# Optimization experiments

Measured on AMD Instinct MI355X. Metric: run time of the kernel, lower is better.

## Reference

```python
import jax, jax.numpy as jnp
import numpy as np
from jax import lax

B, S, D = 4, 2048, 1024
E, F, K = 8, 2816, 2
W_SCALE = 0.02


def setup_inputs() -> dict:
    key = jax.random.key(0)
    ks = jax.random.split(key, 5)
    return {
        "x": jax.random.normal(ks[0], (B, S, D), dtype=jnp.float32),
        "gate_w": jax.random.normal(ks[1], (E, D), dtype=jnp.float32) * W_SCALE,
        "w_gate": jax.random.normal(ks[2], (E, F, D), dtype=jnp.float32) * W_SCALE,
        "w_up": jax.random.normal(ks[3], (E, F, D), dtype=jnp.float32) * W_SCALE,
        "w_down": jax.random.normal(ks[4], (E, D, F), dtype=jnp.float32) * W_SCALE,
    }


def reference(x, gate_w, w_gate, w_up, w_down):
    # Router: logits [B,S,E]
    logits = jnp.einsum("bsd,ed->bse", x, gate_w)
    top_v, top_i = lax.top_k(logits, K)              # [B,S,K]
    top_w = jax.nn.softmax(top_v, axis=-1)           # [B,S,K]
    probs = jax.nn.softmax(logits, axis=-1)
    expert_usage = probs.mean(axis=(0, 1))           # [E]
    aux_loss = ((expert_usage - 1.0 / E) ** 2).sum()

    # Per-token per-expert combine weight: cw[b,s,e] = sum_k top_w[...,k] * 1[top_i[...,k]==e]
    onehot = jax.nn.one_hot(top_i, E, dtype=x.dtype)       # [B,S,K,E]
    cw = jnp.einsum("bsk,bske->ebs", top_w, onehot)        # [E,B,S]

    # Loop (scan) over the small fixed expert axis; each expert: SwiGLU FFN over all
    # tokens, masked/weighted by cw (same math as masked gather + scatter-add combine).
    def body(acc, ew):
        wg, wu, wd, cwe = ew                                # [F,D],[F,D],[D,F],[B,S]
        g = jax.nn.silu(jnp.einsum("bsd,fd->bsf", x, wg))
        u = jnp.einsum("bsd,fd->bsf", x, wu)
        out_e = jnp.einsum("bsf,df->bsd", g * u, wd)
        return acc + cwe[..., None] * out_e, None

    out, _ = lax.scan(body, jnp.zeros_like(x), (w_gate, w_up, w_down, cw))
    return out, aux_loss
```

## Files before the change

### kernel.cpp

```cpp
#include <hip/hip_runtime.h>
#include <hip/hip_bf16.h>
#include <stdint.h>

#define Dd 1024
#define Ee 8
#define Ff 2816
#define Tt 8192
#define Pp 16384

#define BMT 128
#define MAXT 136

using bf16x8 = __attribute__((ext_vector_type(8))) short;
using f32x4  = __attribute__((ext_vector_type(4))) float;
using f4v    = __attribute__((ext_vector_type(4))) float;
using u4v    = __attribute__((ext_vector_type(4))) unsigned int;

__device__ __forceinline__ uint16_t f2bf(float f) {
    union { float f; uint32_t u; } v; v.f = f;
    return (uint16_t)((v.u + 0x7fffu + ((v.u >> 16) & 1u)) >> 16);
}
__device__ __forceinline__ float bf2f(uint16_t b) {
    union { uint32_t u; float f; } v; v.u = (uint32_t)b << 16; return v.f;
}
__device__ __forceinline__ uint32_t pack2(float a, float b) {
    return (uint32_t)f2bf(a) | ((uint32_t)f2bf(b) << 16);
}
__device__ __forceinline__ u4v pack8v(f4v a, f4v b) {
    u4v r; r.x = pack2(a.x, a.y); r.y = pack2(a.z, a.w);
    r.z = pack2(b.x, b.y); r.w = pack2(b.z, b.w); return r;
}
__device__ __forceinline__ int swz(int row, int cb) {
    return row * 128 + (cb ^ ((row & 7) << 4));
}
__device__ __forceinline__ void gload16(const void* g, void* lds) {
    __builtin_amdgcn_global_load_lds(
        (const __attribute__((address_space(1))) uint32_t*)(uintptr_t)g,
        (__attribute__((address_space(3))) uint32_t*)(uintptr_t)lds,
        16, 0, 0);
}

__global__ __launch_bounds__(256) void router_kernel(
    const float* __restrict__ x, const float* __restrict__ gw,
    float* __restrict__ usage_part, int* __restrict__ tok_i,
    float* __restrict__ tok_w, uint16_t* __restrict__ Xb)
{
    __shared__ float usw[4][Ee];
    int tid = threadIdx.x;
    int wave = tid >> 6, lane = tid & 63;
    int t = blockIdx.x * 4 + wave;

    const float* xp = x + (size_t)t * Dd + lane * 16;
    f4v xr0 = *(const f4v*)(xp);
    f4v xr1 = *(const f4v*)(xp + 4);
    f4v xr2 = *(const f4v*)(xp + 8);
    f4v xr3 = *(const f4v*)(xp + 12);

    uint4* dst = (uint4*)(Xb + (size_t)t * Dd + lane * 16);
    u4v p0 = pack8v(xr0, xr1), p1 = pack8v(xr2, xr3);
    dst[0] = *(uint4*)&p0;
    dst[1] = *(uint4*)&p1;

    float logits[Ee];
    #pragma unroll
    for (int e = 0; e < Ee; ++e) {
        const float* gp = gw + e * Dd + lane * 16;
        f4v g0 = *(const f4v*)(gp);
        f4v g1 = *(const f4v*)(gp + 4);
        f4v g2 = *(const f4v*)(gp + 8);
        f4v g3 = *(const f4v*)(gp + 12);
        f4v sv = xr0 * g0 + xr1 * g1 + xr2 * g2 + xr3 * g3;
        float s = sv.x + sv.y + sv.z + sv.w;
        #pragma unroll
        for (int m = 1; m < 64; m <<= 1) s += __shfl_xor(s, m, 64);
        logits[e] = s;
    }
    float v1 = -1e30f, v2 = -1e30f; int i1 = 0, i2 = 0;
    #pragma unroll
    for (int e = 0; e < Ee; ++e) {
        float l = logits[e];
        if (l > v1) { v2 = v1; i2 = i1; v1 = l; i1 = e; }
        else if (l > v2) { v2 = l; i2 = e; }
    }
    float ex2 = expf(v2 - v1);
    float w1 = 1.f / (1.f + ex2);
    float w2 = ex2 * w1;
    float p[Ee]; float se = 0.f;
    #pragma unroll
    for (int e = 0; e < Ee; ++e) { p[e] = expf(logits[e] - v1); se += p[e]; }
    float inv = 1.f / se;
    if (lane == 0) {
        #pragma unroll
        for (int e = 0; e < Ee; ++e) usw[wave][e] = p[e] * inv;
        tok_i[t * 2] = i1; tok_i[t * 2 + 1] = i2;
        tok_w[t * 2] = w1; tok_w[t * 2 + 1] = w2;
    }
    __syncthreads();
    if (tid < Ee)
        usage_part[(size_t)blockIdx.x * Ee + tid] =
            usw[0][tid] + usw[1][tid] + usw[2][tid] + usw[3][tid];
}

__global__ __launch_bounds__(256) void hist_kernel(
    const int* __restrict__ tok_i, int* __restrict__ hist)
{
    __shared__ int h[Ee];
    int tid = threadIdx.x;
    if (tid < Ee) h[tid] = 0;
    __syncthreads();
    int t = blockIdx.x * 256 + tid;
    atomicAdd(&h[tok_i[t * 2]], 1);
    atomicAdd(&h[tok_i[t * 2 + 1]], 1);
    __syncthreads();
    if (tid < Ee) hist[blockIdx.x * Ee + tid] = h[tid];
}

__global__ void scan_kernel(
    const float* __restrict__ usage_part, const int* __restrict__ hist,
    int* __restrict__ seg_off, int* __restrict__ boff, int* __restrict__ ntiles,
    int* __restrict__ tile_e, int* __restrict__ tile_row0, float* __restrict__ out_aux)
{
    __shared__ float us[Ee][32];
    int tid = threadIdx.x;
    int e = tid & 7, sl = tid >> 3;
    float s = 0.f;
    for (int b = sl; b < Tt / 4; b += 32) s += usage_part[(size_t)b * Ee + e];
    us[e][sl] = s;
    __syncthreads();
    if (tid == 0) {
        float aux = 0.f;
        int counts[Ee];
        for (int ee = 0; ee < Ee; ++ee) {
            float u = 0.f;
            for (int k = 0; k < 32; ++k) u += us[ee][k];
            u /= (float)Tt;
            float d = u - 0.125f; aux += d * d;
        }
        *out_aux = aux;
        for (int ee = 0; ee < Ee; ++ee) {
            int c = 0;
            for (int b2 = 0; b2 < 32; ++b2) c += hist[b2 * Ee + ee];
            counts[ee] = c;
        }
        int off = 0;
        for (int ee = 0; ee < Ee; ++ee) { seg_off[ee] = off; off += counts[ee]; }
        seg_off[Ee] = off;
        int cur[Ee];
        for (int ee = 0; ee < Ee; ++ee) cur[ee] = seg_off[ee];
        for (int b2 = 0; b2 < 32; ++b2)
            for (int ee = 0; ee < Ee; ++ee) {
                boff[b2 * Ee + ee] = cur[ee];
                cur[ee] += hist[b2 * Ee + ee];
            }
        int ti = 0;
        for (int ee = 0; ee < Ee; ++ee) {
            int so = seg_off[ee], cnt = counts[ee];
            for (int r = 0; r < cnt; r += BMT) { tile_e[ti] = ee; tile_row0[ti] = so + r; ++ti; }
        }
        *ntiles = ti;
    }
}

__global__ __launch_bounds__(256) void emit_kernel(
    const int* __restrict__ tok_i, const float* __restrict__ tok_w,
    const int* __restrict__ boff, int* __restrict__ token_id,
    float* __restrict__ pair_w, int* __restrict__ pos)
{
    __shared__ int cur[Ee];
    int tid = threadIdx.x;
    if (tid < Ee) cur[tid] = boff[blockIdx.x * Ee + tid];
    __syncthreads();
    int t = blockIdx.x * 256 + tid;
    int i1 = tok_i[t * 2], i2 = tok_i[t * 2 + 1];
    int s1 = atomicAdd(&cur[i1], 1);
    token_id[s1] = t; pair_w[s1] = tok_w[t * 2];     pos[t * 2] = s1;
    int s2 = atomicAdd(&cur[i2], 1);
    token_id[s2] = t; pair_w[s2] = tok_w[t * 2 + 1]; pos[t * 2 + 1] = s2;
}

__global__ __launch_bounds__(256) void conv_all_kernel(
    const float* __restrict__ g, const float* __restrict__ u,
    const float* __restrict__ dsrc, uint16_t* __restrict__ w1b,
    uint16_t* __restrict__ wdb)
{
    int part = blockIdx.x / 1408;
    long long base = (long long)(blockIdx.x - part * 1408) * 16384;
    int tid = threadIdx.x;
    const float* src = (part == 0) ? g : (part == 1) ? u : dsrc;
    f4v v[16];
    #pragma unroll
    for (int j = 0; j < 8; ++j) {
        const float* s = src + base + j * 2048 + tid * 8;
        v[2 * j]     = __builtin_nontemporal_load((const f4v*)s);
        v[2 * j + 1] = __builtin_nontemporal_load((const f4v*)(s + 4));
    }
    __builtin_amdgcn_sched_barrier(0);
    if (part == 2) {
        #pragma unroll
        for (int j = 0; j < 8; ++j) {
            long long ii = base + j * 2048 + tid * 8;
            *(u4v*)(wdb + ii) = pack8v(v[2 * j], v[2 * j + 1]);
        }
    } else {
        int roff = (part == 1) ? 16 : 0;
        #pragma unroll
        for (int j = 0; j < 8; ++j) {
            long long ii = base + j * 2048 + tid * 8;
            int d = (int)(ii & 1023);
            long long row = ii >> 10;
            int e = (int)(row / Ff), f = (int)(row - (long long)e * Ff);
            size_t rg = (size_t)e * 5632 + (size_t)(f >> 4) * 32 + (f & 15) + roff;
            *(u4v*)(w1b + rg * 1024 + d) = pack8v(v[2 * j], v[2 * j + 1]);
        }
    }
}

template<int NKT, int MODE>
__device__ __forceinline__ void gemm_core(
    const uint16_t* __restrict__ Abase, const uint16_t* __restrict__ Bbase,
    const int* __restrict__ seg_off, const int* __restrict__ tile_e,
    const int* __restrict__ tile_row0, const int* __restrict__ ntiles,
    const int* __restrict__ token_id, const float* __restrict__ pair_w,
    uint16_t* __restrict__ hbuf, uint16_t* __restrict__ Pbuf, float* __restrict__ out,
    int tile0, int Tc, int ltr)
{
    constexpr int LD = (MODE == 0) ? Dd : Ff;

    int b = blockIdx.x;
    int nt, lt;
    if constexpr (MODE == 0) {
        int x = b & 7, p = b >> 3;
        nt = p / ltr;
        lt = x * ltr + (p - nt * ltr);
        if (lt >= Tc) return;
    } else {
        nt = b & 7;
        lt = b >> 3;
    }
    int tidx = tile0 + lt;
    if (tidx >= *ntiles) return;
    int e = tile_e[tidx];
    int row0 = tile_row0[tidx];
    int rows = seg_off[e + 1] - row0; if (rows > BMT) rows = BMT;
    int slot = lt * BMT;

    __shared__ uint4 lds4[32768 / 16];
    char* smA = (char*)lds4;
    char* smB = smA + 16384;

    int tid = threadIdx.x, lane = tid & 63, wv = tid >> 6;
    int wr = wv >> 1, wc = wv & 1;

    int srow = wv * 32 + (lane >> 3);
    int csw = ((lane & 7) ^ (lane >> 3)) * 8;
    const uint16_t* aPs[4];
    const uint16_t* bP;
    if constexpr (MODE == 0) {
        #pragma unroll
        for (int i = 0; i < 4; ++i) {
            int pr = row0 + srow + i * 8;
            if (pr > Pp - 1) pr = Pp - 1;
            aPs[i] = Abase + (size_t)token_id[pr] * Dd + csw;
        }
        bP = Bbase + ((size_t)e * 5632 + nt * 128 + srow) * LD + csw;
    } else {
        const uint16_t* aP0 = Abase + (size_t)(slot + srow) * LD + csw;
        #pragma unroll
        for (int i = 0; i < 4; ++i) aPs[i] = aP0 + (size_t)(i * 8) * LD;
        bP = Bbase + ((size_t)e * Dd + nt * 128 + srow) * LD + csw;
    }
    char* aL = smA + wv * 4096;
    char* bL = smB + wv * 4096;

    f32x4 acc[4][4];
    f32x4 zero4 = {0.f, 0.f, 0.f, 0.f};
    #pragma unroll
    for (int m = 0; m < 4; ++m)
        #pragma unroll
        for (int n = 0; n < 4; ++n) acc[m][n] = zero4;

    #pragma unroll 1
    for (int kt = 0; kt < NKT; ++kt) {
        #pragma unroll
        for (int i = 0; i < 4; ++i) {
            gload16(aPs[i] + kt * 64, aL + i * 1024);
            gload16(bP + (size_t)(i * 8) * LD + kt * 64, bL + i * 1024);
        }
        __syncthreads();
        #pragma unroll
        for (int kk = 0; kk < 2; ++kk) {
            int cb = kk * 64 + ((lane >> 4) << 4);
            bf16x8 a[4], bfr[4];
            #pragma unroll
            for (int m = 0; m < 4; ++m)
                a[m] = *(const bf16x8*)(smA + swz(wr * 64 + m * 16 + (lane & 15), cb));
            #pragma unroll
            for (int n = 0; n < 4; ++n)
                bfr[n] = *(const bf16x8*)(smB + swz(wc * 64 + n * 16 + (lane & 15), cb));
            #pragma unroll
            for (int m = 0; m < 4; ++m)
                #pragma unroll
                for (int n = 0; n < 4; ++n)
                    acc[m][n] = __builtin_amdgcn_mfma_f32_16x16x32_bf16(a[m], bfr[n], acc[m][n], 0, 0, 0);
        }
        __syncthreads();
    }

    if constexpr (MODE == 0) {
        int hc = nt * 64 + wc * 32 + (lane & 15);
        #pragma unroll
        for (int m = 0; m < 4; ++m) {
            #pragma unroll
            for (int g = 0; g < 4; ++g) {
                int rr = wr * 64 + m * 16 + (lane >> 4) * 4 + g;
                if (rr < rows) {
                    uint16_t* hp = hbuf + (size_t)(slot + rr) * Ff + hc;
                    float g0 = acc[m][0][g], u0 = acc[m][1][g];
                    hp[0]  = f2bf(g0 * u0 / (1.f + expf(-g0)));
                    float g1 = acc[m][2][g], u1 = acc[m][3][g];
                    hp[16] = f2bf(g1 * u1 / (1.f + expf(-g1)));
                }
            }
        }
    } else if constexpr (MODE == 1) {
        int col = nt * 128 + wc * 64 + (lane & 15);
        #pragma unroll
        for (int m = 0; m < 4; ++m) {
            #pragma unroll
            for (int g = 0; g < 4; ++g) {
                int rr = wr * 64 + m * 16 + (lane >> 4) * 4 + g;
                if (rr < rows) {
                    uint16_t* pp = Pbuf + (size_t)(row0 + rr) * Dd + col;
                    pp[0]  = f2bf(acc[m][0][g]);
                    pp[16] = f2bf(acc[m][1][g]);
                    pp[32] = f2bf(acc[m][2][g]);
                    pp[48] = f2bf(acc[m][3][g]);
                }
            }
        }
    } else {
        int col = nt * 128 + wc * 64 + (lane & 15);
        #pragma unroll
        for (int m = 0; m < 4; ++m) {
            #pragma unroll
            for (int g = 0; g < 4; ++g) {
                int rr = wr * 64 + m * 16 + (lane >> 4) * 4 + g;
                if (rr < rows) {
                    int pr = row0 + rr;
                    int tok = token_id[pr];
                    float w = pair_w[pr];
                    float* op = out + (size_t)tok * Dd + col;
                    atomicAdd(op + 0,  w * acc[m][0][g]);
                    atomicAdd(op + 16, w * acc[m][1][g]);
                    atomicAdd(op + 32, w * acc[m][2][g]);
                    atomicAdd(op + 48, w * acc[m][3][g]);
                }
            }
        }
    }
}

#define GEMM_ARGS const uint16_t* __restrict__ Abase, const uint16_t* __restrict__ Bbase, \
    const int* __restrict__ seg_off, const int* __restrict__ tile_e, \
    const int* __restrict__ tile_row0, const int* __restrict__ ntiles, \
    const int* __restrict__ token_id, const float* __restrict__ pair_w, \
    uint16_t* __restrict__ hbuf, uint16_t* __restrict__ Pbuf, float* __restrict__ out, \
    int tile0, int Tc, int ltr
#define GEMM_PASS Abase, Bbase, seg_off, tile_e, tile_row0, ntiles, token_id, pair_w, \
    hbuf, Pbuf, out, tile0, Tc, ltr

__global__ __launch_bounds__(256, 3) void gemm1_kernel(GEMM_ARGS) {
    gemm_core<16, 0>(GEMM_PASS);
}
__global__ __launch_bounds__(256, 3) void gemm2p_kernel(GEMM_ARGS) {
    gemm_core<44, 1>(GEMM_PASS);
}
__global__ __launch_bounds__(256, 3) void gemm2a_kernel(GEMM_ARGS) {
    gemm_core<44, 2>(GEMM_PASS);
}

__global__ __launch_bounds__(256) void combine_kernel(
    const uint16_t* __restrict__ P, const int* __restrict__ pos,
    const float* __restrict__ tok_w, float* __restrict__ out)
{
    int t = blockIdx.x;
    int d = threadIdx.x * 4;
    int s1 = pos[t * 2], s2 = pos[t * 2 + 1];
    float w1 = tok_w[t * 2], w2 = tok_w[t * 2 + 1];
    uint2 pa = *(const uint2*)(P + (size_t)s1 * Dd + d);
    uint2 pb = *(const uint2*)(P + (size_t)s2 * Dd + d);
    f4v o;
    o.x = w1 * bf2f((uint16_t)(pa.x & 0xffff))  + w2 * bf2f((uint16_t)(pb.x & 0xffff));
    o.y = w1 * bf2f((uint16_t)(pa.x >> 16))     + w2 * bf2f((uint16_t)(pb.x >> 16));
    o.z = w1 * bf2f((uint16_t)(pa.y & 0xffff))  + w2 * bf2f((uint16_t)(pb.y & 0xffff));
    o.w = w1 * bf2f((uint16_t)(pa.y >> 16))     + w2 * bf2f((uint16_t)(pb.y >> 16));
    *(f4v*)(out + (size_t)t * Dd + d) = o;
}

extern "C" void kernel_launch(void* const* d_in, const int* in_sizes, int n_in,
                              void* d_out, int out_size, void* d_ws, size_t ws_size,
                              hipStream_t stream)
{
    const float* x     = (const float*)d_in[0];
    const float* gw    = (const float*)d_in[1];
    const float* wgate = (const float*)d_in[2];
    const float* wup   = (const float*)d_in[3];
    const float* wdown = (const float*)d_in[4];
    float* out = (float*)d_out;

    char* ws = (char*)d_ws;
    float* usage_part = (float*)(ws);
    int*   hist       = (int*)(ws + 65536);
    int*   seg_off    = (int*)(ws + 66560);
    int*   boff       = (int*)(ws + 66624);
    int*   ntiles     = (int*)(ws + 67648);
    int*   tile_e     = (int*)(ws + 67712);
    int*   tile_row0  = (int*)(ws + 68736);
    int*   tok_i      = (int*)(ws + 73728);
    float* tok_w      = (float*)(ws + 139264);
    int*   token_id   = (int*)(ws + 204800);
    float* pair_w     = (float*)(ws + 270336);
    int*   pos        = (int*)(ws + 335872);
    const size_t CTRL  = 401408;
    const size_t TILEB = (size_t)BMT * Ff * 2;
    const size_t XbB   = (size_t)Tt * Dd * 2;
    const size_t W1B   = 2ull * Ee * Ff * Dd * 2;
    const size_t WDB   = (size_t)Ee * Dd * Ff * 2;
    const size_t PB    = (size_t)Pp * Dd * 2;

    size_t fixed = CTRL + XbB + W1B + WDB;
    if (ws_size < fixed + TILEB) {
        hipMemsetAsync(d_out, 0, (size_t)out_size * 4, stream);
        return;
    }

    uint16_t* Xb   = (uint16_t*)(ws + CTRL);
    uint16_t* W1b  = (uint16_t*)(ws + CTRL + XbB);
    uint16_t* wd_b = (uint16_t*)(ws + CTRL + XbB + W1B);
    size_t rem = ws_size - fixed;

    router_kernel<<<Tt / 4, 256, 0, stream>>>(x, gw, usage_part, tok_i, tok_w, Xb);
    hist_kernel<<<Tt / 256, 256, 0, stream>>>(tok_i, hist);
    scan_kernel<<<1, 256, 0, stream>>>(usage_part, hist, seg_off, boff,
                                       ntiles, tile_e, tile_row0, out + (out_size - 1));
    emit_kernel<<<Tt / 256, 256, 0, stream>>>(tok_i, tok_w, boff, token_id, pair_w, pos);
    conv_all_kernel<<<3 * 1408, 256, 0, stream>>>(wgate, wup, wdown, W1b, wd_b);

    int TcP = (rem > PB) ? (int)((rem - PB) / TILEB) : 0;
    if (TcP > MAXT) TcP = MAXT;
    bool useP = (TcP >= 24);
    uint16_t* Pbuf = nullptr;
    uint16_t* hbuf;
    int Tc;
    if (useP) {
        Pbuf = (uint16_t*)(ws + fixed);
        hbuf = (uint16_t*)(ws + fixed + PB);
        Tc = TcP;
    } else {
        hbuf = (uint16_t*)(ws + fixed);
        Tc = (int)(rem / TILEB);
        if (Tc > MAXT) Tc = MAXT;
        hipMemsetAsync(d_out, 0, (size_t)(out_size - 1) * 4, stream);
    }
    int nchunks = (MAXT + Tc - 1) / Tc;
    Tc = (MAXT + nchunks - 1) / nchunks;

    int ltr = (Tc + 7) / 8;
    int nwg1 = 8 * ltr * 44;
    int nwg2 = Tc * 8;
    for (int c = 0; c < nchunks; ++c) {
        int tile0 = c * Tc;
        gemm1_kernel<<<nwg1, 256, 0, stream>>>(
            Xb, W1b, seg_off, tile_e, tile_row0, ntiles, token_id, pair_w,
            hbuf, Pbuf, out, tile0, Tc, ltr);
        if (useP) {
            gemm2p_kernel<<<nwg2, 256, 0, stream>>>(
                hbuf, wd_b, seg_off, tile_e, tile_row0, ntiles, token_id, pair_w,
                hbuf, Pbuf, out, tile0, Tc, ltr);
        } else {
            gemm2a_kernel<<<nwg2, 256, 0, stream>>>(
                hbuf, wd_b, seg_off, tile_e, tile_row0, ntiles, token_id, pair_w,
                hbuf, Pbuf, out, tile0, Tc, ltr);
        }
    }
    if (useP)
        combine_kernel<<<Tt, 256, 0, stream>>>(Pbuf, pos, tok_w, out);
}
```

Baseline: 487.5 us.

## Fuse router, histogram and weight conversion; overlap down-proj conversion with GEMM1

The router and histogram kernels are merged into one prep kernel, which also runs the gate/up weight bf16 conversion in extra blocks, so there are fewer launches and the memory-bound conversion runs alongside routing. The down-projection weight conversion moves into extra blocks of the first GEMM1 launch so it can overlap with compute. The scan kernel now reduces the finer per-block histograms into 32 groups in parallel, and the workspace layout is enlarged to match. This adds coupling between stages. It relies on GEMM1 blocks finishing before gemm2 reads wd_b, which kernel ordering on the stream guarantees.

```diff
diff --git a/kernel.cpp b/kernel.cpp
--- a/kernel.cpp
+++ b/kernel.cpp
@@ -40,15 +40,70 @@
         16, 0, 0);
 }
 
-__global__ __launch_bounds__(256) void router_kernel(
+__device__ __forceinline__ void conv_w1_body(
+    const float* __restrict__ src, uint16_t* __restrict__ w1b, int roff, int blk)
+{
+    long long base = (long long)blk * 16384;
+    int tid = threadIdx.x;
+    f4v v[16];
+    #pragma unroll
+    for (int j = 0; j < 8; ++j) {
+        const float* s = src + base + j * 2048 + tid * 8;
+        v[2 * j]     = __builtin_nontemporal_load((const f4v*)s);
+        v[2 * j + 1] = __builtin_nontemporal_load((const f4v*)(s + 4));
+    }
+    __builtin_amdgcn_sched_barrier(0);
+    #pragma unroll
+    for (int j = 0; j < 8; ++j) {
+        long long ii = base + j * 2048 + tid * 8;
+        int d = (int)(ii & 1023);
+        long long row = ii >> 10;
+        int e = (int)(row / Ff), f = (int)(row - (long long)e * Ff);
+        size_t rg = (size_t)e * 5632 + (size_t)(f >> 4) * 32 + (f & 15) + roff;
+        *(u4v*)(w1b + rg * 1024 + d) = pack8v(v[2 * j], v[2 * j + 1]);
+    }
+}
+__device__ __forceinline__ void conv_wd_body(
+    const float* __restrict__ src, uint16_t* __restrict__ wdb, int blk)
+{
+    long long base = (long long)blk * 16384;
+    int tid = threadIdx.x;
+    f4v v[16];
+    #pragma unroll
+    for (int j = 0; j < 8; ++j) {
+        const float* s = src + base + j * 2048 + tid * 8;
+        v[2 * j]     = __builtin_nontemporal_load((const f4v*)s);
+        v[2 * j + 1] = __builtin_nontemporal_load((const f4v*)(s + 4));
+    }
+    __builtin_amdgcn_sched_barrier(0);
+    #pragma unroll
+    for (int j = 0; j < 8; ++j) {
+        long long ii = base + j * 2048 + tid * 8;
+        *(u4v*)(wdb + ii) = pack8v(v[2 * j], v[2 * j + 1]);
+    }
+}
+
+__global__ __launch_bounds__(256) void prep_kernel(
     const float* __restrict__ x, const float* __restrict__ gw,
-    float* __restrict__ usage_part, int* __restrict__ tok_i,
+    const float* __restrict__ wgate, const float* __restrict__ wup,
+    uint16_t* __restrict__ W1b, float* __restrict__ usage_part,
+    int* __restrict__ hist, int* __restrict__ tok_i,
     float* __restrict__ tok_w, uint16_t* __restrict__ Xb)
 {
+    if (blockIdx.x < 2816) {
+        int part = blockIdx.x / 1408;
+        conv_w1_body(part ? wup : wgate, W1b, part ? 16 : 0,
+                     blockIdx.x - part * 1408);
+        return;
+    }
+    int bid = blockIdx.x - 2816;
     __shared__ float usw[4][Ee];
+    __shared__ int h[Ee];
     int tid = threadIdx.x;
+    if (tid < Ee) h[tid] = 0;
+    __syncthreads();
     int wave = tid >> 6, lane = tid & 63;
-    int t = blockIdx.x * 4 + wave;
+    int t = bid * 4 + wave;
 
     const float* xp = x + (size_t)t * Dd + lane * 16;
     f4v xr0 = *(const f4v*)(xp);
@@ -94,25 +149,15 @@
         for (int e = 0; e < Ee; ++e) usw[wave][e] = p[e] * inv;
         tok_i[t * 2] = i1; tok_i[t * 2 + 1] = i2;
         tok_w[t * 2] = w1; tok_w[t * 2 + 1] = w2;
+        atomicAdd(&h[i1], 1);
+        atomicAdd(&h[i2], 1);
     }
     __syncthreads();
-    if (tid < Ee)
-        usage_part[(size_t)blockIdx.x * Ee + tid] =
+    if (tid < Ee) {
+        usage_part[(size_t)bid * Ee + tid] =
             usw[0][tid] + usw[1][tid] + usw[2][tid] + usw[3][tid];
-}
-
-__global__ __launch_bounds__(256) void hist_kernel(
-    const int* __restrict__ tok_i, int* __restrict__ hist)
-{
-    __shared__ int h[Ee];
-    int tid = threadIdx.x;
-    if (tid < Ee) h[tid] = 0;
-    __syncthreads();
-    int t = blockIdx.x * 256 + tid;
-    atomicAdd(&h[tok_i[t * 2]], 1);
-    atomicAdd(&h[tok_i[t * 2 + 1]], 1);
-    __syncthreads();
-    if (tid < Ee) hist[blockIdx.x * Ee + tid] = h[tid];
+        hist[bid * Ee + tid] = h[tid];
+    }
 }
 
 __global__ void scan_kernel(
@@ -121,11 +166,20 @@
     int* __restrict__ tile_e, int* __restrict__ tile_row0, float* __restrict__ out_aux)
 {
     __shared__ float us[Ee][32];
+    __shared__ int gh[32][Ee];
     int tid = threadIdx.x;
-    int e = tid & 7, sl = tid >> 3;
-    float s = 0.f;
-    for (int b = sl; b < Tt / 4; b += 32) s += usage_part[(size_t)b * Ee + e];
-    us[e][sl] = s;
+    {
+        int e = tid & 7, sl = tid >> 3;
+        float s = 0.f;
+        for (int b = sl; b < 2048; b += 32) s += usage_part[(size_t)b * Ee + e];
+        us[e][sl] = s;
+    }
+    {
+        int g = tid >> 3, e = tid & 7;
+        int s = 0;
+        for (int rb = g * 64; rb < g * 64 + 64; ++rb) s += hist[rb * Ee + e];
+        gh[g][e] = s;
+    }
     __syncthreads();
     if (tid == 0) {
         float aux = 0.f;
@@ -139,7 +193,7 @@
         *out_aux = aux;
         for (int ee = 0; ee < Ee; ++ee) {
             int c = 0;
-            for (int b2 = 0; b2 < 32; ++b2) c += hist[b2 * Ee + ee];
+            for (int g = 0; g < 32; ++g) c += gh[g][ee];
             counts[ee] = c;
         }
         int off = 0;
@@ -147,10 +201,10 @@
         seg_off[Ee] = off;
         int cur[Ee];
         for (int ee = 0; ee < Ee; ++ee) cur[ee] = seg_off[ee];
-        for (int b2 = 0; b2 < 32; ++b2)
+        for (int g = 0; g < 32; ++g)
             for (int ee = 0; ee < Ee; ++ee) {
-                boff[b2 * Ee + ee] = cur[ee];
-                cur[ee] += hist[b2 * Ee + ee];
+                boff[g * Ee + ee] = cur[ee];
+                cur[ee] += gh[g][ee];
             }
         int ti = 0;
         for (int ee = 0; ee < Ee; ++ee) {
@@ -178,45 +232,9 @@
     token_id[s2] = t; pair_w[s2] = tok_w[t * 2 + 1]; pos[t * 2 + 1] = s2;
 }
 
-__global__ __launch_bounds__(256) void conv_all_kernel(
-    const float* __restrict__ g, const float* __restrict__ u,
-    const float* __restrict__ dsrc, uint16_t* __restrict__ w1b,
-    uint16_t* __restrict__ wdb)
-{
-    int part = blockIdx.x / 1408;
-    long long base = (long long)(blockIdx.x - part * 1408) * 16384;
-    int tid = threadIdx.x;
-    const float* src = (part == 0) ? g : (part == 1) ? u : dsrc;
-    f4v v[16];
-    #pragma unroll
-    for (int j = 0; j < 8; ++j) {
-        const float* s = src + base + j * 2048 + tid * 8;
-        v[2 * j]     = __builtin_nontemporal_load((const f4v*)s);
-        v[2 * j + 1] = __builtin_nontemporal_load((const f4v*)(s + 4));
-    }
-    __builtin_amdgcn_sched_barrier(0);
-    if (part == 2) {
-        #pragma unroll
-        for (int j = 0; j < 8; ++j) {
-            long long ii = base + j * 2048 + tid * 8;
-            *(u4v*)(wdb + ii) = pack8v(v[2 * j], v[2 * j + 1]);
-        }
-    } else {
-        int roff = (part == 1) ? 16 : 0;
-        #pragma unroll
-        for (int j = 0; j < 8; ++j) {
-            long long ii = base + j * 2048 + tid * 8;
-            int d = (int)(ii & 1023);
-            long long row = ii >> 10;
-            int e = (int)(row / Ff), f = (int)(row - (long long)e * Ff);
-            size_t rg = (size_t)e * 5632 + (size_t)(f >> 4) * 32 + (f & 15) + roff;
-            *(u4v*)(w1b + rg * 1024 + d) = pack8v(v[2 * j], v[2 * j + 1]);
-        }
-    }
-}
-
 template<int NKT, int MODE>
 __device__ __forceinline__ void gemm_core(
+    int b,
     const uint16_t* __restrict__ Abase, const uint16_t* __restrict__ Bbase,
     const int* __restrict__ seg_off, const int* __restrict__ tile_e,
     const int* __restrict__ tile_row0, const int* __restrict__ ntiles,
@@ -226,7 +244,6 @@
 {
     constexpr int LD = (MODE == 0) ? Dd : Ff;
 
-    int b = blockIdx.x;
     int nt, lt;
     if constexpr (MODE == 0) {
         int x = b & 7, p = b >> 3;
@@ -369,14 +386,20 @@
 #define GEMM_PASS Abase, Bbase, seg_off, tile_e, tile_row0, ntiles, token_id, pair_w, \
     hbuf, Pbuf, out, tile0, Tc, ltr
 
-__global__ __launch_bounds__(256, 3) void gemm1_kernel(GEMM_ARGS) {
-    gemm_core<16, 0>(GEMM_PASS);
+__global__ __launch_bounds__(256, 3) void gemm1_kernel(
+    GEMM_ARGS, const float* __restrict__ wdown, uint16_t* __restrict__ wd_b, int nwg1)
+{
+    if ((int)blockIdx.x >= nwg1) {
+        conv_wd_body(wdown, wd_b, (int)blockIdx.x - nwg1);
+        return;
+    }
+    gemm_core<16, 0>((int)blockIdx.x, GEMM_PASS);
 }
 __global__ __launch_bounds__(256, 3) void gemm2p_kernel(GEMM_ARGS) {
-    gemm_core<44, 1>(GEMM_PASS);
+    gemm_core<44, 1>((int)blockIdx.x, GEMM_PASS);
 }
 __global__ __launch_bounds__(256, 3) void gemm2a_kernel(GEMM_ARGS) {
-    gemm_core<44, 2>(GEMM_PASS);
+    gemm_core<44, 2>((int)blockIdx.x, GEMM_PASS);
 }
 
 __global__ __launch_bounds__(256) void combine_kernel(
@@ -411,17 +434,17 @@
     char* ws = (char*)d_ws;
     float* usage_part = (float*)(ws);
     int*   hist       = (int*)(ws + 65536);
-    int*   seg_off    = (int*)(ws + 66560);
-    int*   boff       = (int*)(ws + 66624);
-    int*   ntiles     = (int*)(ws + 67648);
-    int*   tile_e     = (int*)(ws + 67712);
-    int*   tile_row0  = (int*)(ws + 68736);
-    int*   tok_i      = (int*)(ws + 73728);
-    float* tok_w      = (float*)(ws + 139264);
-    int*   token_id   = (int*)(ws + 204800);
-    float* pair_w     = (float*)(ws + 270336);
-    int*   pos        = (int*)(ws + 335872);
-    const size_t CTRL  = 401408;
+    int*   seg_off    = (int*)(ws + 131072);
+    int*   boff       = (int*)(ws + 131200);
+    int*   ntiles     = (int*)(ws + 132224);
+    int*   tile_e     = (int*)(ws + 132288);
+    int*   tile_row0  = (int*)(ws + 133312);
+    int*   tok_i      = (int*)(ws + 139264);
+    float* tok_w      = (float*)(ws + 204800);
+    int*   token_id   = (int*)(ws + 270336);
+    float* pair_w     = (float*)(ws + 335872);
+    int*   pos        = (int*)(ws + 401408);
+    const size_t CTRL  = 466944;
     const size_t TILEB = (size_t)BMT * Ff * 2;
     const size_t XbB   = (size_t)Tt * Dd * 2;
     const size_t W1B   = 2ull * Ee * Ff * Dd * 2;
@@ -439,12 +462,11 @@
     uint16_t* wd_b = (uint16_t*)(ws + CTRL + XbB + W1B);
     size_t rem = ws_size - fixed;
 
-    router_kernel<<<Tt / 4, 256, 0, stream>>>(x, gw, usage_part, tok_i, tok_w, Xb);
-    hist_kernel<<<Tt / 256, 256, 0, stream>>>(tok_i, hist);
+    prep_kernel<<<4864, 256, 0, stream>>>(x, gw, wgate, wup, W1b,
+                                          usage_part, hist, tok_i, tok_w, Xb);
     scan_kernel<<<1, 256, 0, stream>>>(usage_part, hist, seg_off, boff,
                                        ntiles, tile_e, tile_row0, out + (out_size - 1));
-    emit_kernel<<<Tt / 256, 256, 0, stream>>>(tok_i, tok_w, boff, token_id, pair_w, pos);
-    conv_all_kernel<<<3 * 1408, 256, 0, stream>>>(wgate, wup, wdown, W1b, wd_b);
+    emit_kernel<<<32, 256, 0, stream>>>(tok_i, tok_w, boff, token_id, pair_w, pos);
 
     int TcP = (rem > PB) ? (int)((rem - PB) / TILEB) : 0;
     if (TcP > MAXT) TcP = MAXT;
@@ -470,9 +492,10 @@
     int nwg2 = Tc * 8;
     for (int c = 0; c < nchunks; ++c) {
         int tile0 = c * Tc;
-        gemm1_kernel<<<nwg1, 256, 0, stream>>>(
+        int extra = (c == 0) ? 1408 : 0;
+        gemm1_kernel<<<nwg1 + extra, 256, 0, stream>>>(
             Xb, W1b, seg_off, tile_e, tile_row0, ntiles, token_id, pair_w,
-            hbuf, Pbuf, out, tile0, Tc, ltr);
+            hbuf, Pbuf, out, tile0, Tc, ltr, wdown, wd_b, nwg1);
         if (useP) {
             gemm2p_kernel<<<nwg2, 256, 0, stream>>>(
                 hbuf, wd_b, seg_off, tile_e, tile_row0, ntiles, token_id, pair_w,
```

Result: faster. 474.8 us (median of 2 runs) (-2.6%).
